# Kernel tuning notes

Measured on AMD Instinct MI355X. Metric: run time of the kernel, lower is better.

Reference implementation:

```python
import jax, jax.numpy as jnp
import numpy as np

DIM, NHEAD, DM, DL = 512, 8, 64, 128
B, N = 8, 4096


def setup_inputs() -> dict:
    key = jax.random.key(0)
    ks = jax.random.split(key, 6)
    x = jax.random.normal(ks[0], (B, N, DIM), jnp.float32)
    std1 = 1.0 / np.sqrt(DL * DIM).astype(np.float32)
    V = jax.random.uniform(ks[1], (DM, DL), jnp.float32, -std1, std1)
    std2 = np.float32(1.0 / np.sqrt(DL))
    W = jax.random.uniform(ks[2], (NHEAD, DL), jnp.float32, -std2, std2)
    std3 = np.float32(1.0 / np.sqrt(NHEAD * DIM * DM))
    WX = jax.random.uniform(ks[3], (NHEAD, DIM, DM), jnp.float32, -std3, std3)
    std4 = np.float32(1.0 / np.sqrt(DM * DL))
    gate_w = jax.random.uniform(ks[4], (DIM, DL), jnp.float32, -std4, std4)
    # number of valid instances per bag, in [N//2, N]
    true_num = jax.random.randint(ks[5], (B,), N // 2, N + 1)
    return {"x": x, "WX": WX, "V": V, "W": W, "gate_w": gate_w, "true_num": true_num}


def reference(x, WX, V, W, gate_w, true_num):
    Bv, Nv, _ = x.shape
    # per-head instance projections: (H, B, N, dm)
    mh = jnp.einsum('bnd,hdm->hbnm', x, WX)
    # gate is computed from x (identical across heads in the original expand) -> compute once
    gate = jax.nn.sigmoid(jnp.einsum('bnd,dl->bnl', x, gate_w))  # (B, N, dl)
    # gated tanh similarity, then contract with per-head attention vector W
    dis = jnp.tanh(jnp.einsum('hbnm,ml->hbnl', mh, V)) * gate[None]  # (H, B, N, dl)
    scores = jnp.einsum('hbnl,hl->hbn', dis, W)  # (H, B, N)
    # mask out padded instances (index >= true_num[b])
    valid = jnp.arange(Nv)[None, :] < true_num[:, None]  # (B, N)
    scores = jnp.where(valid[None], scores, jnp.float32(-1e20))
    soft = jax.nn.softmax(scores, axis=2)  # (H, B, N)
    # attention-weighted pooling per head, then concat heads: (B, H*dm)
    feat = jnp.einsum('hbn,hbnm->bhm', soft, mh).reshape(Bv, -1)
    return feat, soft[0]
```

## Files before the change

### kernel.cpp

```cpp
#include <hip/hip_runtime.h>
#include <hip/hip_bf16.h>

#define DIM   512
#define NHEAD 8
#define DM    64
#define DL    128
#define BBAG  8
#define NINST 4096
#define MTOT  (BBAG*NINST)
#define NBLK  (MTOT/64)

typedef short   bf16x8 __attribute__((ext_vector_type(8)));
typedef __bf16  bf16v8 __attribute__((ext_vector_type(8)));
typedef float   f32x4  __attribute__((ext_vector_type(4)));
typedef short   s16x4  __attribute__((ext_vector_type(4)));

__device__ __forceinline__ short f2b(float f) {
  __hip_bfloat16 h = __float2bfloat16(f);
  return __builtin_bit_cast(short, h);
}
__device__ __forceinline__ float b2f(short s) {
  __hip_bfloat16 h = __builtin_bit_cast(__hip_bfloat16, s);
  return __bfloat162float(h);
}
__device__ __forceinline__ f32x4 mfma_bf16(bf16x8 a, bf16x8 b, f32x4 c) {
  return __builtin_amdgcn_mfma_f32_16x16x32_bf16(
      __builtin_bit_cast(bf16v8, a), __builtin_bit_cast(bf16v8, b), c, 0, 0, 0);
}
__device__ __forceinline__ float fast_tanh(float x) {
  float t = __expf(2.0f * x);
  return 1.0f - 2.0f * __builtin_amdgcn_rcpf(t + 1.0f);
}
__device__ __forceinline__ float fast_sigmoid(float x) {
  return __builtin_amdgcn_rcpf(1.0f + __expf(-x));
}

__global__ __launch_bounds__(256) void prep_weights(
    const float* __restrict__ WX, const float* __restrict__ V,
    const float* __restrict__ gate_w,
    short* __restrict__ Wt2, short* __restrict__ Vt_f) {
  __shared__ float lds[32 * 129];
  const int bid = blockIdx.x, t = threadIdx.x;

  if (bid < 128) {
    const int h = bid >> 4, ks = bid & 15;
    {
      const int kl = t >> 3, m8 = (t & 7) * 8;
      const float* src = WX + ((size_t)(h * DIM + ks * 32 + kl) * DM + m8);
      #pragma unroll
      for (int j = 0; j < 8; ++j) lds[kl * 129 + m8 + j] = src[j];
    }
    __syncthreads();
    {
      const int m = t >> 2, q = t & 3;
      const int col = h * 64 + m;
      const int q2 = (q + ((col & 15) >> 1)) & 3;
      short* dst = Wt2 + ks * 20480 + col * 32 + q2 * 8;
      #pragma unroll
      for (int j = 0; j < 8; ++j) dst[j] = f2b(lds[(q * 8 + j) * 129 + m]);
    }
  } else if (bid < 144) {
    const int ks = bid - 128;
    #pragma unroll
    for (int rep = 0; rep < 2; ++rep) {
      const int idx = rep * 2048 + t * 8;
      const int kl = idx >> 7, l8 = idx & 127;
      const float* src = gate_w + ((size_t)(ks * 32 + kl) * DL + l8);
      #pragma unroll
      for (int j = 0; j < 8; ++j) lds[kl * 129 + l8 + j] = src[j];
    }
    __syncthreads();
    #pragma unroll
    for (int rep = 0; rep < 2; ++rep) {
      const int piece = rep * 256 + t;
      const int l = piece >> 2, q = piece & 3;
      const int col = 512 + l;
      const int q2 = (q + ((col & 15) >> 1)) & 3;
      short* dst = Wt2 + ks * 20480 + col * 32 + q2 * 8;
      #pragma unroll
      for (int j = 0; j < 8; ++j) dst[j] = f2b(lds[(q * 8 + j) * 129 + l]);
    }
  } else {
    #pragma unroll
    for (int rep = 0; rep < 4; ++rep) {
      const int e = t + rep * 256;
      const int ct = e >> 7, half = (e >> 6) & 1, lane = e & 63;
      const int r = lane & 15, q = lane >> 4;
      short* dst = Vt_f + (size_t)e * 8;
      #pragma unroll
      for (int j = 0; j < 8; ++j) {
        const int m = half * 32 + q * 8 + j;
        dst[j] = f2b(V[(size_t)m * DL + ct * 16 + r]);
      }
    }
  }
}

#define BLOAD(dst, addr) \
  asm volatile("global_load_dwordx4 %0, %1, off" : "=v"(dst) : "v"(addr))

__global__ __launch_bounds__(512) void fused_kernel(
    const float* __restrict__ x, const short* __restrict__ Wt2,
    const short* __restrict__ Vt_f, const float* __restrict__ W,
    const int* __restrict__ true_num,
    float* __restrict__ part, float* __restrict__ esum,
    float* __restrict__ e0) {
  __shared__ alignas(16) short lds[40960];
  const int tid = threadIdx.x;
  const int blk = blockIdx.x;
  const int bm0 = blk * 64;
  const int lane = tid & 63;
  const int w = tid >> 6;
  const int r = lane & 15;
  const int q = lane >> 4;
  const int swzs = (q + (r >> 1)) & 3;
  char* lda = reinterpret_cast<char*>(lds);
  char* mh_base = reinterpret_cast<char*>(lds);
  short* gate_lds = lds + 32768;

  const int tn = true_num[blk >> 6];
  const int nbase = bm0 & (NINST - 1);

  {
    const int arow = tid >> 3, ap = tid & 7;
    const int aslot = ((ap >> 1) + ((arow & 15) >> 1)) & 3;
    const float* asrc = x + ((size_t)(bm0 + arow) << 9) + (ap << 2);
    char* adst = lda + arow * 64 + aslot * 16 + (ap & 1) * 8;
    #pragma unroll
    for (int ks = 0; ks < 16; ++ks) {
      f32x4 v = *reinterpret_cast<const f32x4*>(asrc + ks * 32);
      s16x4 sv; sv.x = f2b(v[0]); sv.y = f2b(v[1]); sv.z = f2b(v[2]); sv.w = f2b(v[3]);
      *reinterpret_cast<s16x4*>(adst + ks * 4096) = sv;
    }
  }
  __syncthreads();

  const short* bbase = Wt2 + (80 * w + r) * 32 + swzs * 8;
  bf16x8 bufs[3][5];
  #pragma unroll
  for (int ct = 0; ct < 5; ++ct) BLOAD(bufs[0][ct], bbase + 0 * 20480 + ct * 512);
  #pragma unroll
  for (int ct = 0; ct < 5; ++ct) BLOAD(bufs[1][ct], bbase + 1 * 20480 + ct * 512);

  const int aoff = r * 64 + swzs * 16;
  bf16x8 afb[2][4];
  #pragma unroll
  for (int rt = 0; rt < 4; ++rt)
    afb[0][rt] = *reinterpret_cast<const bf16x8*>(lda + 0 * 4096 + aoff + rt * 1024);

  f32x4 acc[4][5];
  #pragma unroll
  for (int rt = 0; rt < 4; ++rt)
    #pragma unroll
    for (int ct = 0; ct < 5; ++ct) acc[rt][ct] = f32x4{0.f, 0.f, 0.f, 0.f};

  #pragma unroll
  for (int ks = 0; ks < 16; ++ks) {
    if (ks + 2 < 16) {
      #pragma unroll
      for (int ct = 0; ct < 5; ++ct)
        BLOAD(bufs[(ks + 2) % 3][ct], bbase + (ks + 2) * 20480 + ct * 512);
    }
    if (ks < 14)      asm volatile("s_waitcnt vmcnt(10)" ::: "memory");
    else if (ks < 15) asm volatile("s_waitcnt vmcnt(5)" ::: "memory");
    else              asm volatile("s_waitcnt vmcnt(0)" ::: "memory");
    __builtin_amdgcn_sched_barrier(0);

    if (ks + 1 < 16) {
      #pragma unroll
      for (int rt = 0; rt < 4; ++rt)
        afb[(ks + 1) & 1][rt] = *reinterpret_cast<const bf16x8*>(
            lda + (ks + 1) * 4096 + aoff + rt * 1024);
    }
    #pragma unroll
    for (int ct = 0; ct < 5; ++ct)
      #pragma unroll
      for (int rt = 0; rt < 4; ++rt)
        acc[rt][ct] = mfma_bf16(afb[ks & 1][rt], bufs[ks % 3][ct], acc[rt][ct]);
  }

  __syncthreads();

  #pragma unroll
  for (int rt = 0; rt < 4; ++rt) {
    #pragma unroll
    for (int ct = 0; ct < 5; ++ct) {
      const int colbase = 80 * w + 16 * ct;
      if (colbase < NHEAD * DM) {
        const int col = colbase + r;
        #pragma unroll
        for (int j = 0; j < 4; ++j) {
          const int row = 16 * rt + 4 * q + j;
          const int intra = (col * 2) ^ ((row & 7) << 4);
          *reinterpret_cast<short*>(mh_base + row * 1024 + intra) =
              f2b(acc[rt][ct][j]);
        }
      } else {
        const int ltile = 5 * w + ct - 32;
        s16x4 gv;
        gv.x = f2b(fast_sigmoid(acc[rt][ct][0]));
        gv.y = f2b(fast_sigmoid(acc[rt][ct][1]));
        gv.z = f2b(fast_sigmoid(acc[rt][ct][2]));
        gv.w = f2b(fast_sigmoid(acc[rt][ct][3]));
        *reinterpret_cast<s16x4*>(
            gate_lds + ((rt * 8 + ltile) * 64 + lane) * 4) = gv;
      }
    }
  }
  __syncthreads();

  const int h = w;
  float wc[8];
  #pragma unroll
  for (int lt = 0; lt < 8; ++lt) wc[lt] = W[(size_t)h * DL + 16 * lt + r];

  bf16x8 a0[4], a1[4];
  #pragma unroll
  for (int rt = 0; rt < 4; ++rt) {
    const int row = 16 * rt + r;
    const int swz = (row & 7) << 4;
    a0[rt] = *reinterpret_cast<const bf16x8*>(
        mh_base + row * 1024 + ((h * 128 + q * 16) ^ swz));
    a1[rt] = *reinterpret_cast<const bf16x8*>(
        mh_base + row * 1024 + ((h * 128 + q * 16 + 64) ^ swz));
  }

  float sc[4][4];
  #pragma unroll
  for (int rt = 0; rt < 4; ++rt)
    #pragma unroll
    for (int j = 0; j < 4; ++j) sc[rt][j] = 0.f;

  #pragma unroll
  for (int lt = 0; lt < 8; ++lt) {
    bf16x8 b0 = *reinterpret_cast<const bf16x8*>(Vt_f + (size_t)(lt * 2) * 512 + lane * 8);
    bf16x8 b1 = *reinterpret_cast<const bf16x8*>(Vt_f + (size_t)(lt * 2 + 1) * 512 + lane * 8);
    #pragma unroll
    for (int rt = 0; rt < 4; ++rt) {
      f32x4 t = f32x4{0.f, 0.f, 0.f, 0.f};
      t = mfma_bf16(a0[rt], b0, t);
      t = mfma_bf16(a1[rt], b1, t);
      s16x4 ga = *reinterpret_cast<const s16x4*>(
          gate_lds + ((rt * 8 + lt) * 64 + lane) * 4);
      #pragma unroll
      for (int j = 0; j < 4; ++j) {
        float g = b2f((j == 0) ? ga.x : (j == 1) ? ga.y : (j == 2) ? ga.z : ga.w);
        sc[rt][j] += fast_tanh(t[j]) * g * wc[lt];
      }
    }
  }

  float evals[4] = {0.f, 0.f, 0.f, 0.f};
  float epart = 0.f;
  #pragma unroll
  for (int rt = 0; rt < 4; ++rt) {
    #pragma unroll
    for (int j = 0; j < 4; ++j) {
      sc[rt][j] += __shfl_xor(sc[rt][j], 1);
      sc[rt][j] += __shfl_xor(sc[rt][j], 2);
      sc[rt][j] += __shfl_xor(sc[rt][j], 4);
      sc[rt][j] += __shfl_xor(sc[rt][j], 8);
    }
    if (r < 4) {
      const int row = 16 * rt + 4 * q + r;
      float s = (r == 0) ? sc[rt][0] : (r == 1) ? sc[rt][1]
              : (r == 2) ? sc[rt][2] : sc[rt][3];
      float e = (nbase + row < tn) ? __expf(s) : 0.0f;
      evals[rt] = e;
      epart += e;
      if (w == 0) e0[bm0 + row] = e;
    }
  }
  #pragma unroll
  for (int m = 1; m < 64; m <<= 1) epart += __shfl_xor(epart, m);
  if (lane == 0) esum[(size_t)h * NBLK + blk] = epart;

  {
    float P = 0.f;
    #pragma unroll
    for (int rt = 0; rt < 4; ++rt) {
      #pragma unroll
      for (int rr = 0; rr < 16; ++rr) {
        const int row = 16 * rt + rr;
        const float ev = __shfl(evals[rt], 16 * (rr >> 2) + (rr & 3));
        const int intra = (h * 128 + lane * 2) ^ ((row & 7) << 4);
        P += ev * b2f(*reinterpret_cast<const short*>(mh_base + row * 1024 + intra));
      }
    }
    part[((size_t)h * NBLK + blk) * 64 + lane] = P;
  }
}

__global__ __launch_bounds__(256) void finalize_kernel(
    const float* __restrict__ part, const float* __restrict__ esum,
    const float* __restrict__ e0,
    float* __restrict__ out_feat, float* __restrict__ out_soft) {
  const int h = blockIdx.x >> 3, b = blockIdx.x & 7;
  const int tid = threadIdx.x;

  float Z = 0.f;
  #pragma unroll 8
  for (int c = 0; c < 64; ++c) Z += esum[(size_t)h * NBLK + b * 64 + c];
  const float invZ = 1.0f / Z;

  if (tid < 64) {
    float s = 0.f;
    #pragma unroll 8
    for (int c = 0; c < 64; ++c)
      s += part[((size_t)h * NBLK + b * 64 + c) * 64 + tid];
    out_feat[(size_t)b * (NHEAD * DM) + h * DM + tid] = s * invZ;
  }
  if (h == 0) {
    #pragma unroll
    for (int i = 0; i < 16; ++i) {
      const int n = tid + i * 256;
      out_soft[(size_t)b * NINST + n] = e0[(size_t)b * NINST + n] * invZ;
    }
  }
}

extern "C" void kernel_launch(void* const* d_in, const int* in_sizes, int n_in,
                              void* d_out, int out_size, void* d_ws, size_t ws_size,
                              hipStream_t stream) {
  (void)in_sizes; (void)n_in; (void)out_size; (void)ws_size;
  const float* x      = (const float*)d_in[0];
  const float* WX     = (const float*)d_in[1];
  const float* V      = (const float*)d_in[2];
  const float* W      = (const float*)d_in[3];
  const float* gate_w = (const float*)d_in[4];
  const int* true_num = (const int*)d_in[5];
  float* out = (float*)d_out;

  char* ws = (char*)d_ws;
  short* Wt2  = (short*)ws;  ws += (size_t)(NHEAD * DM + DL) * DIM * 2;
  short* Vt_f = (short*)ws;  ws += (size_t)DL * DM * 2;
  float* part = (float*)ws;  ws += (size_t)NHEAD * NBLK * 64 * 4;
  float* esum = (float*)ws;  ws += (size_t)NHEAD * NBLK * 4;
  float* e0   = (float*)ws;  ws += (size_t)MTOT * 4;

  prep_weights<<<dim3(145), dim3(256), 0, stream>>>(WX, V, gate_w, Wt2, Vt_f);
  fused_kernel<<<dim3(NBLK), dim3(512), 0, stream>>>(
      x, Wt2, Vt_f, W, true_num, part, esum, e0);
  finalize_kernel<<<dim3(NHEAD * BBAG), dim3(256), 0, stream>>>(
      part, esum, e0, out, out + BBAG * NHEAD * DM);
}
```

Measured before the change: 67.84 us.

## Stream x tiles into LDS inside the K loop instead of a prologue

Replaces the upfront load-convert-store of the whole 64x512 x tile with a rolling three-deep register prefetch. Each K-slice is converted to bf16 and written to LDS one step ahead of its use, so the global x loads overlap with MFMA work and the B-operand prefetch. The cost is a workgroup barrier plus an lgkmcnt wait on every K iteration, and hand-tuned vmcnt counts that must exactly match the number of outstanding loads.

```diff
diff --git a/kernel.cpp b/kernel.cpp
--- a/kernel.cpp
+++ b/kernel.cpp
@@ -121,29 +121,34 @@
   const int tn = true_num[blk >> 6];
   const int nbase = bm0 & (NINST - 1);
 
-  {
-    const int arow = tid >> 3, ap = tid & 7;
-    const int aslot = ((ap >> 1) + ((arow & 15) >> 1)) & 3;
-    const float* asrc = x + ((size_t)(bm0 + arow) << 9) + (ap << 2);
-    char* adst = lda + arow * 64 + aslot * 16 + (ap & 1) * 8;
-    #pragma unroll
-    for (int ks = 0; ks < 16; ++ks) {
-      f32x4 v = *reinterpret_cast<const f32x4*>(asrc + ks * 32);
-      s16x4 sv; sv.x = f2b(v[0]); sv.y = f2b(v[1]); sv.z = f2b(v[2]); sv.w = f2b(v[3]);
-      *reinterpret_cast<s16x4*>(adst + ks * 4096) = sv;
-    }
-  }
-  __syncthreads();
+  const int arow = tid >> 3, ap = tid & 7;
+  const int aslot = ((ap >> 1) + ((arow & 15) >> 1)) & 3;
+  const float* asrc = x + ((size_t)(bm0 + arow) << 9) + (ap << 2);
+  char* adst = lda + arow * 64 + aslot * 16 + (ap & 1) * 8;
+
+  f32x4 bufsA[3];
+  auto writeA = [&](f32x4 v, int s) {
+    s16x4 sv; sv.x = f2b(v[0]); sv.y = f2b(v[1]); sv.z = f2b(v[2]); sv.w = f2b(v[3]);
+    *reinterpret_cast<s16x4*>(adst + s * 4096) = sv;
+  };
 
   const short* bbase = Wt2 + (80 * w + r) * 32 + swzs * 8;
   bf16x8 bufs[3][5];
-  #pragma unroll
-  for (int ct = 0; ct < 5; ++ct) BLOAD(bufs[0][ct], bbase + 0 * 20480 + ct * 512);
-  #pragma unroll
-  for (int ct = 0; ct < 5; ++ct) BLOAD(bufs[1][ct], bbase + 1 * 20480 + ct * 512);
-
   const int aoff = r * 64 + swzs * 16;
   bf16x8 afb[2][4];
+
+  BLOAD(bufsA[0], asrc + 0 * 32);
+  BLOAD(bufsA[1], asrc + 1 * 32);
+  BLOAD(bufsA[2], asrc + 2 * 32);
+  #pragma unroll
+  for (int ct = 0; ct < 5; ++ct) BLOAD(bufs[0][ct], bbase + 0 * 20480 + ct * 512);
+  #pragma unroll
+  for (int ct = 0; ct < 5; ++ct) BLOAD(bufs[1][ct], bbase + 1 * 20480 + ct * 512);
+  asm volatile("s_waitcnt vmcnt(12)" ::: "memory");
+  __builtin_amdgcn_sched_barrier(0);
+  writeA(bufsA[0], 0);
+  asm volatile("s_waitcnt lgkmcnt(0)" ::: "memory");
+  __builtin_amdgcn_s_barrier();
   #pragma unroll
   for (int rt = 0; rt < 4; ++rt)
     afb[0][rt] = *reinterpret_cast<const bf16x8*>(lda + 0 * 4096 + aoff + rt * 1024);
@@ -156,16 +161,22 @@
 
   #pragma unroll
   for (int ks = 0; ks < 16; ++ks) {
+    if (ks + 3 < 16) BLOAD(bufsA[(ks + 3) % 3], asrc + (ks + 3) * 32);
     if (ks + 2 < 16) {
       #pragma unroll
       for (int ct = 0; ct < 5; ++ct)
         BLOAD(bufs[(ks + 2) % 3][ct], bbase + (ks + 2) * 20480 + ct * 512);
     }
-    if (ks < 14)      asm volatile("s_waitcnt vmcnt(10)" ::: "memory");
-    else if (ks < 15) asm volatile("s_waitcnt vmcnt(5)" ::: "memory");
-    else              asm volatile("s_waitcnt vmcnt(0)" ::: "memory");
+    if (ks == 0)       asm volatile("s_waitcnt vmcnt(11)" ::: "memory");
+    else if (ks <= 12) asm volatile("s_waitcnt vmcnt(12)" ::: "memory");
+    else if (ks == 13) asm volatile("s_waitcnt vmcnt(11)" ::: "memory");
+    else if (ks == 14) asm volatile("s_waitcnt vmcnt(5)" ::: "memory");
+    else               asm volatile("s_waitcnt vmcnt(0)" ::: "memory");
     __builtin_amdgcn_sched_barrier(0);
 
+    if (ks + 1 < 16) writeA(bufsA[(ks + 1) % 3], ks + 1);
+    asm volatile("s_waitcnt lgkmcnt(0)" ::: "memory");
+    __builtin_amdgcn_s_barrier();
     if (ks + 1 < 16) {
       #pragma unroll
       for (int rt = 0; rt < 4; ++rt)
```

New measurement: 64.60 us. 1.05x faster.

## Halve rows per block to 32 and shrink pipeline buffers for occupancy

Applied to the files above, without the earlier changes.

Cuts the row tile of the fused kernel from 64 to 32 rows. This halves the LDS footprint and the accumulator and A-fragment registers, and launch_bounds is raised to request 4 blocks per CU. The B-operand prefetch goes from triple to double buffering, with loads issued after the MFMAs, and the x staging is rewritten for the new tile shape. The aim is higher occupancy and more blocks to spread across CUs, at the cost of twice as many blocks each re-reading the full weight matrix, shallower prefetch, and twice the partials for finalize to reduce.

```diff
diff --git a/kernel.cpp b/kernel.cpp
--- a/kernel.cpp
+++ b/kernel.cpp
@@ -8,7 +8,9 @@
 #define BBAG  8
 #define NINST 4096
 #define MTOT  (BBAG*NINST)
-#define NBLK  (MTOT/64)
+#define BM    32
+#define NBLK  (MTOT/BM)
+#define CPB   (NBLK/BBAG)
 
 typedef short   bf16x8 __attribute__((ext_vector_type(8)));
 typedef __bf16  bf16v8 __attribute__((ext_vector_type(8)));
@@ -99,16 +101,16 @@
 #define BLOAD(dst, addr) \
   asm volatile("global_load_dwordx4 %0, %1, off" : "=v"(dst) : "v"(addr))
 
-__global__ __launch_bounds__(512) void fused_kernel(
+__global__ __launch_bounds__(512, 4) void fused_kernel(
     const float* __restrict__ x, const short* __restrict__ Wt2,
     const short* __restrict__ Vt_f, const float* __restrict__ W,
     const int* __restrict__ true_num,
     float* __restrict__ part, float* __restrict__ esum,
     float* __restrict__ e0) {
-  __shared__ alignas(16) short lds[40960];
+  __shared__ alignas(16) short lds[18432];
   const int tid = threadIdx.x;
   const int blk = blockIdx.x;
-  const int bm0 = blk * 64;
+  const int bm0 = blk * BM;
   const int lane = tid & 63;
   const int w = tid >> 6;
   const int r = lane & 15;
@@ -116,73 +118,73 @@
   const int swzs = (q + (r >> 1)) & 3;
   char* lda = reinterpret_cast<char*>(lds);
   char* mh_base = reinterpret_cast<char*>(lds);
-  short* gate_lds = lds + 32768;
-
-  const int tn = true_num[blk >> 6];
+  short* gate_lds = lds + 16384;
+
+  const int tn = true_num[blk >> 7];
   const int nbase = bm0 & (NINST - 1);
 
   {
-    const int arow = tid >> 3, ap = tid & 7;
-    const int aslot = ((ap >> 1) + ((arow & 15) >> 1)) & 3;
-    const float* asrc = x + ((size_t)(bm0 + arow) << 9) + (ap << 2);
-    char* adst = lda + arow * 64 + aslot * 16 + (ap & 1) * 8;
+    const int arow = tid >> 4, ap = tid & 15;
+    const int aslot = ((ap >> 2) + ((arow & 15) >> 1)) & 3;
+    const float* asrc = x + ((size_t)(bm0 + arow) << 9) + ap * 2;
+    char* adst = lda + arow * 64 + aslot * 16 + (ap & 3) * 4;
     #pragma unroll
     for (int ks = 0; ks < 16; ++ks) {
-      f32x4 v = *reinterpret_cast<const f32x4*>(asrc + ks * 32);
-      s16x4 sv; sv.x = f2b(v[0]); sv.y = f2b(v[1]); sv.z = f2b(v[2]); sv.w = f2b(v[3]);
-      *reinterpret_cast<s16x4*>(adst + ks * 4096) = sv;
+      float2 v = *reinterpret_cast<const float2*>(asrc + ks * 32);
+      unsigned pk = ((unsigned)(unsigned short)f2b(v.y) << 16) |
+                    (unsigned)(unsigned short)f2b(v.x);
+      *reinterpret_cast<unsigned*>(adst + ks * 2048) = pk;
     }
   }
   __syncthreads();
 
   const short* bbase = Wt2 + (80 * w + r) * 32 + swzs * 8;
-  bf16x8 bufs[3][5];
+  bf16x8 bufs[2][5];
   #pragma unroll
   for (int ct = 0; ct < 5; ++ct) BLOAD(bufs[0][ct], bbase + 0 * 20480 + ct * 512);
   #pragma unroll
   for (int ct = 0; ct < 5; ++ct) BLOAD(bufs[1][ct], bbase + 1 * 20480 + ct * 512);
 
   const int aoff = r * 64 + swzs * 16;
-  bf16x8 afb[2][4];
-  #pragma unroll
-  for (int rt = 0; rt < 4; ++rt)
-    afb[0][rt] = *reinterpret_cast<const bf16x8*>(lda + 0 * 4096 + aoff + rt * 1024);
-
-  f32x4 acc[4][5];
-  #pragma unroll
-  for (int rt = 0; rt < 4; ++rt)
+  bf16x8 afb[2][2];
+  #pragma unroll
+  for (int rt = 0; rt < 2; ++rt)
+    afb[0][rt] = *reinterpret_cast<const bf16x8*>(lda + 0 * 2048 + aoff + rt * 1024);
+
+  f32x4 acc[2][5];
+  #pragma unroll
+  for (int rt = 0; rt < 2; ++rt)
     #pragma unroll
     for (int ct = 0; ct < 5; ++ct) acc[rt][ct] = f32x4{0.f, 0.f, 0.f, 0.f};
 
   #pragma unroll
   for (int ks = 0; ks < 16; ++ks) {
+    if (ks < 15) asm volatile("s_waitcnt vmcnt(5)" ::: "memory");
+    else         asm volatile("s_waitcnt vmcnt(0)" ::: "memory");
+    __builtin_amdgcn_sched_barrier(0);
+
+    if (ks + 1 < 16) {
+      #pragma unroll
+      for (int rt = 0; rt < 2; ++rt)
+        afb[(ks + 1) & 1][rt] = *reinterpret_cast<const bf16x8*>(
+            lda + (ks + 1) * 2048 + aoff + rt * 1024);
+    }
+    #pragma unroll
+    for (int ct = 0; ct < 5; ++ct)
+      #pragma unroll
+      for (int rt = 0; rt < 2; ++rt)
+        acc[rt][ct] = mfma_bf16(afb[ks & 1][rt], bufs[ks & 1][ct], acc[rt][ct]);
     if (ks + 2 < 16) {
       #pragma unroll
       for (int ct = 0; ct < 5; ++ct)
-        BLOAD(bufs[(ks + 2) % 3][ct], bbase + (ks + 2) * 20480 + ct * 512);
-    }
-    if (ks < 14)      asm volatile("s_waitcnt vmcnt(10)" ::: "memory");
-    else if (ks < 15) asm volatile("s_waitcnt vmcnt(5)" ::: "memory");
-    else              asm volatile("s_waitcnt vmcnt(0)" ::: "memory");
-    __builtin_amdgcn_sched_barrier(0);
-
-    if (ks + 1 < 16) {
-      #pragma unroll
-      for (int rt = 0; rt < 4; ++rt)
-        afb[(ks + 1) & 1][rt] = *reinterpret_cast<const bf16x8*>(
-            lda + (ks + 1) * 4096 + aoff + rt * 1024);
-    }
-    #pragma unroll
-    for (int ct = 0; ct < 5; ++ct)
-      #pragma unroll
-      for (int rt = 0; rt < 4; ++rt)
-        acc[rt][ct] = mfma_bf16(afb[ks & 1][rt], bufs[ks % 3][ct], acc[rt][ct]);
+        BLOAD(bufs[ks & 1][ct], bbase + (ks + 2) * 20480 + ct * 512);
+    }
   }
 
   __syncthreads();
 
   #pragma unroll
-  for (int rt = 0; rt < 4; ++rt) {
+  for (int rt = 0; rt < 2; ++rt) {
     #pragma unroll
     for (int ct = 0; ct < 5; ++ct) {
       const int colbase = 80 * w + 16 * ct;
@@ -214,9 +216,9 @@
   #pragma unroll
   for (int lt = 0; lt < 8; ++lt) wc[lt] = W[(size_t)h * DL + 16 * lt + r];
 
-  bf16x8 a0[4], a1[4];
-  #pragma unroll
-  for (int rt = 0; rt < 4; ++rt) {
+  bf16x8 a0[2], a1[2];
+  #pragma unroll
+  for (int rt = 0; rt < 2; ++rt) {
     const int row = 16 * rt + r;
     const int swz = (row & 7) << 4;
     a0[rt] = *reinterpret_cast<const bf16x8*>(
@@ -225,9 +227,9 @@
         mh_base + row * 1024 + ((h * 128 + q * 16 + 64) ^ swz));
   }
 
-  float sc[4][4];
-  #pragma unroll
-  for (int rt = 0; rt < 4; ++rt)
+  float sc[2][4];
+  #pragma unroll
+  for (int rt = 0; rt < 2; ++rt)
     #pragma unroll
     for (int j = 0; j < 4; ++j) sc[rt][j] = 0.f;
 
@@ -236,7 +238,7 @@
     bf16x8 b0 = *reinterpret_cast<const bf16x8*>(Vt_f + (size_t)(lt * 2) * 512 + lane * 8);
     bf16x8 b1 = *reinterpret_cast<const bf16x8*>(Vt_f + (size_t)(lt * 2 + 1) * 512 + lane * 8);
     #pragma unroll
-    for (int rt = 0; rt < 4; ++rt) {
+    for (int rt = 0; rt < 2; ++rt) {
       f32x4 t = f32x4{0.f, 0.f, 0.f, 0.f};
       t = mfma_bf16(a0[rt], b0, t);
       t = mfma_bf16(a1[rt], b1, t);
@@ -250,10 +252,10 @@
     }
   }
 
-  float evals[4] = {0.f, 0.f, 0.f, 0.f};
+  float evals[2] = {0.f, 0.f};
   float epart = 0.f;
   #pragma unroll
-  for (int rt = 0; rt < 4; ++rt) {
+  for (int rt = 0; rt < 2; ++rt) {
     #pragma unroll
     for (int j = 0; j < 4; ++j) {
       sc[rt][j] += __shfl_xor(sc[rt][j], 1);
@@ -278,7 +280,7 @@
   {
     float P = 0.f;
     #pragma unroll
-    for (int rt = 0; rt < 4; ++rt) {
+    for (int rt = 0; rt < 2; ++rt) {
       #pragma unroll
       for (int rr = 0; rr < 16; ++rr) {
         const int row = 16 * rt + rr;
@@ -300,14 +302,14 @@
 
   float Z = 0.f;
   #pragma unroll 8
-  for (int c = 0; c < 64; ++c) Z += esum[(size_t)h * NBLK + b * 64 + c];
+  for (int c = 0; c < CPB; ++c) Z += esum[(size_t)h * NBLK + b * CPB + c];
   const float invZ = 1.0f / Z;
 
   if (tid < 64) {
     float s = 0.f;
     #pragma unroll 8
-    for (int c = 0; c < 64; ++c)
-      s += part[((size_t)h * NBLK + b * 64 + c) * 64 + tid];
+    for (int c = 0; c < CPB; ++c)
+      s += part[((size_t)h * NBLK + b * CPB + c) * 64 + tid];
     out_feat[(size_t)b * (NHEAD * DM) + h * DM + tid] = s * invZ;
   }
   if (h == 0) {
```

After: 64.94 us, median of 2. -4.3%, faster.
